# Optimization experiments

Hardware: AMD Instinct MI355X
Metric: run time of the kernel (lower is better)

## Reference

```python
import jax, jax.numpy as jnp
import numpy as np
from jax import lax

LAG = 0.5  # lag_constant

def setup_inputs() -> dict:
    key = jax.random.key(0)
    ks = jax.random.split(key, 8)
    B, T, D, H, O = 64, 512, 256, 1024, 256
    return {
        "obs_seq": jax.random.normal(ks[0], (B, T, D), dtype=jnp.float32),
        "h0": jax.random.normal(ks[1], (B, H), dtype=jnp.float32),
        "W_in": jax.random.normal(ks[2], (H, D), dtype=jnp.float32) * (1.0 / np.sqrt(D)),
        "b_in": jax.random.normal(ks[3], (H,), dtype=jnp.float32) * 0.01,
        "W_h": jax.random.normal(ks[4], (H, H), dtype=jnp.float32) * (1.0 / np.sqrt(H)),
        "b_h": jax.random.normal(ks[5], (H,), dtype=jnp.float32) * 0.01,
        "W_out": jax.random.normal(ks[6], (O, H), dtype=jnp.float32) * (1.0 / np.sqrt(H)),
        "b_out": jax.random.normal(ks[7], (O,), dtype=jnp.float32) * 0.01,
    }

def reference(obs_seq, h0, W_in, b_in, W_h, b_h, W_out, b_out):
    # obs_seq: [B, T, D]; scan over time with hard sequential dependency on h.
    def step(h, obs_t):  # h: [B,H], obs_t: [B,D]
        pre = obs_t @ W_in.T + b_in + h @ W_h.T + b_h
        h_new = LAG * jax.nn.relu(pre) + (1.0 - LAG) * h
        out = h_new @ W_out.T + b_out  # [B,O]
        return h_new, (out, h_new)

    obs_tbd = jnp.swapaxes(obs_seq, 0, 1)  # [T,B,D]
    _, (outs, hs) = lax.scan(step, h0, obs_tbd)
    # stack along seq_dim=1 as in the original
    return jnp.swapaxes(outs, 0, 1), jnp.swapaxes(hs, 0, 1)
```

## Files before the change

kernel.cpp:

```cpp
#include <hip/hip_runtime.h>
#include <cstddef>


static constexpr int Bb = 64;
static constexpr int Tt = 512;
static constexpr int Dd = 256;
static constexpr int Hh = 1024;
static constexpr int Oo = 256;

typedef __attribute__((ext_vector_type(8))) short bf16x8;
typedef __attribute__((ext_vector_type(4))) float f32x4;
typedef unsigned long long ull;

static __device__ __forceinline__ unsigned short f2b(float f) {
    unsigned int u = __float_as_uint(f);
    u = (u + 0x7fffu + ((u >> 16) & 1u)) >> 16;
    return (unsigned short)u;
}
static __device__ __forceinline__ ull pack4(float a, float b, float c, float d) {
    return (ull)f2b(a) | ((ull)f2b(b) << 16) | ((ull)f2b(c) << 32) | ((ull)f2b(d) << 48);
}

static __device__ __forceinline__ int hla_base(int r) {
    return ((r >> 5) << 7) + (((r >> 3) & 3) << 3) + (r & 7);
}
static __device__ __forceinline__ int hla_addr(int r, int m) {
    return hla_base(r) + (m << 5);
}

__global__ __launch_bounds__(256) void gemm_bt_kernel(const float* __restrict__ A,
                                                      const float* __restrict__ Bt,
                                                      const float* __restrict__ bias1,
                                                      const float* __restrict__ bias2,
                                                      float* __restrict__ C,
                                                      int M, int N, int K)
{
    __shared__ float As[128 * 17];
    __shared__ float Bs[128 * 17];
    const int tid = threadIdx.x;
    const int nTiles = N >> 7;
    const int mt = blockIdx.x / nTiles;
    const int nt = blockIdx.x - mt * nTiles;
    const int m0 = mt << 7, n0 = nt << 7;
    const int tx = tid & 15, ty = tid >> 4;

    const int row = tid >> 1;
    const int c8  = (tid & 1) << 3;

    float acc[8][8] = {};

    for (int kt = 0; kt < K; kt += 16) {
        const float4 a0 = *(const float4*)&A [(size_t)(m0 + row) * K + kt + c8];
        const float4 a1 = *(const float4*)&A [(size_t)(m0 + row) * K + kt + c8 + 4];
        const float4 b0 = *(const float4*)&Bt[(size_t)(n0 + row) * K + kt + c8];
        const float4 b1 = *(const float4*)&Bt[(size_t)(n0 + row) * K + kt + c8 + 4];
        __syncthreads();
        {
            const int ab = row * 17 + c8;
            As[ab + 0] = a0.x; As[ab + 1] = a0.y; As[ab + 2] = a0.z; As[ab + 3] = a0.w;
            As[ab + 4] = a1.x; As[ab + 5] = a1.y; As[ab + 6] = a1.z; As[ab + 7] = a1.w;
            Bs[ab + 0] = b0.x; Bs[ab + 1] = b0.y; Bs[ab + 2] = b0.z; Bs[ab + 3] = b0.w;
            Bs[ab + 4] = b1.x; Bs[ab + 5] = b1.y; Bs[ab + 6] = b1.z; Bs[ab + 7] = b1.w;
        }
        __syncthreads();
#pragma unroll
        for (int kk = 0; kk < 16; ++kk) {
            float af[8], bf[8];
#pragma unroll
            for (int i = 0; i < 8; ++i) af[i] = As[(ty * 8 + i) * 17 + kk];
#pragma unroll
            for (int j = 0; j < 4; ++j) bf[j] = Bs[(tx * 4 + j) * 17 + kk];
#pragma unroll
            for (int j = 0; j < 4; ++j) bf[4 + j] = Bs[(64 + tx * 4 + j) * 17 + kk];
#pragma unroll
            for (int i = 0; i < 8; ++i) {
#pragma unroll
                for (int j = 0; j < 8; ++j) {
                    acc[i][j] = fmaf(af[i], bf[j], acc[i][j]);
                }
            }
        }
    }

    float bs[8];
#pragma unroll
    for (int j = 0; j < 4; ++j) {
        const int n1 = n0 + tx * 4 + j;
        const int n2 = n0 + 64 + tx * 4 + j;
        bs[j]     = bias1[n1] + (bias2 ? bias2[n1] : 0.0f);
        bs[4 + j] = bias1[n2] + (bias2 ? bias2[n2] : 0.0f);
    }
#pragma unroll
    for (int i = 0; i < 8; ++i) {
        const int m = m0 + ty * 8 + i;
        float4 v0 = make_float4(acc[i][0] + bs[0], acc[i][1] + bs[1],
                                acc[i][2] + bs[2], acc[i][3] + bs[3]);
        float4 v1 = make_float4(acc[i][4] + bs[4], acc[i][5] + bs[5],
                                acc[i][6] + bs[6], acc[i][7] + bs[7]);
        *(float4*)&C[(size_t)m * N + n0 + tx * 4]      = v0;
        *(float4*)&C[(size_t)m * N + n0 + 64 + tx * 4] = v1;
    }
}

__global__ __launch_bounds__(512, 2) void rnn_kernel(float* __restrict__ Xhs,
                                                     const float* __restrict__ h0,
                                                     const float* __restrict__ Wh,
                                                     ull* __restrict__ hx)
{
    __shared__ short hlA[2][32 * 128];

    const int tid  = threadIdx.x;
    const int bid  = blockIdx.x;
    const int team = bid & 15;
    const int wg   = bid >> 4;
    const int r0   = wg << 7;
    const int b0   = team << 2;

    const int lane = tid & 63;
    const int wv   = tid >> 6;

    bf16x8 wfrag[32];
    {
        const float* wrow = Wh + (size_t)(r0 + wv * 16 + (lane & 15)) * Hh + ((lane >> 4) << 3);
#pragma unroll
        for (int s = 0; s < 32; ++s) {
            const float4 lo = *(const float4*)(wrow + s * 32);
            const float4 hi = *(const float4*)(wrow + s * 32 + 4);
            bf16x8 w;
            w[0] = (short)f2b(lo.x); w[1] = (short)f2b(lo.y);
            w[2] = (short)f2b(lo.z); w[3] = (short)f2b(lo.w);
            w[4] = (short)f2b(hi.x); w[5] = (short)f2b(hi.y);
            w[6] = (short)f2b(hi.z); w[7] = (short)f2b(hi.w);
            wfrag[s] = w;
        }
    }

#pragma unroll
    for (int it = 0; it < 2; ++it) {
        const int idx = it * 512 + tid;
        const int b   = idx >> 8;
        const int k0  = (idx & 255) << 2;
        const float4 v = *(const float4*)&h0[(size_t)(b0 + b) * Hh + k0];
        *(ull*)&hlA[0][hla_addr(k0, b)] = pack4(v.x, v.y, v.z, v.w);
    }

    const int npair = (tid < 384) ? 2 : 1;
    int soff[2], sbase[2];
#pragma unroll
    for (int j = 0; j < 2; ++j) {
        int q = tid + j * 512; if (q >= 896) q = 0;
        const int wr = q >> 7;
        const int rl = q & 127;
        const int wi = wr + ((wr >= wg) ? 1 : 0);
        soff[j]  = (wi << 8) + (rl << 1);
        sbase[j] = hla_base((wi << 7) + rl);
    }

    const bool ex    = (lane < 16);
    const int  exrow = r0 + wv * 16 + lane;
    const int  sb    = hla_base(exrow);
    float hprev[4] = {0.f, 0.f, 0.f, 0.f};
    if (ex) {
#pragma unroll
        for (int i = 0; i < 4; ++i)
            hprev[i] = h0[(size_t)(b0 + i) * Hh + exrow];
    }
    __syncthreads();

    const int aoff = (lane & 3) * 32 + ((lane >> 4) << 3);

    for (int t = 0; t < Tt; ++t) {
        const short* hc = hlA[t & 1];
        short*       hn = hlA[(t + 1) & 1];

        float xr[4] = {0.f, 0.f, 0.f, 0.f};
        if (ex) {
#pragma unroll
            for (int i = 0; i < 4; ++i)
                xr[i] = Xhs[((size_t)(b0 + i) * Tt + t) * Hh + exrow];
        }

        f32x4 acc0 = {0.f, 0.f, 0.f, 0.f}, acc1 = acc0, acc2 = acc0, acc3 = acc0;
#pragma unroll
        for (int s = 0; s < 32; s += 4) {
            acc0 = __builtin_amdgcn_mfma_f32_16x16x32_bf16(
                       *(const bf16x8*)(hc + (s + 0) * 128 + aoff), wfrag[s + 0], acc0, 0, 0, 0);
            acc1 = __builtin_amdgcn_mfma_f32_16x16x32_bf16(
                       *(const bf16x8*)(hc + (s + 1) * 128 + aoff), wfrag[s + 1], acc1, 0, 0, 0);
            acc2 = __builtin_amdgcn_mfma_f32_16x16x32_bf16(
                       *(const bf16x8*)(hc + (s + 2) * 128 + aoff), wfrag[s + 2], acc2, 0, 0, 0);
            acc3 = __builtin_amdgcn_mfma_f32_16x16x32_bf16(
                       *(const bf16x8*)(hc + (s + 3) * 128 + aoff), wfrag[s + 3], acc3, 0, 0, 0);
        }
        const f32x4 accs01 = acc0 + acc1;
        const f32x4 accs23 = acc2 + acc3;
        const f32x4 acc    = accs01 + accs23;

        float hnew[4] = {0.f, 0.f, 0.f, 0.f};
        unsigned short hb[4] = {0, 0, 0, 0};
        if (ex) {
#pragma unroll
            for (int i = 0; i < 4; ++i) {
                const float pre = acc[i] + xr[i];
                hnew[i]  = 0.5f * fmaxf(pre, 0.0f) + 0.5f * hprev[i];
                hprev[i] = hnew[i];
                hb[i]    = f2b(hnew[i]);
            }
        }

        if (t + 1 < Tt) {
            ull* __restrict__ slab =
                hx + (size_t)(((t + 1) & 1) * 16 + team) * (8 * 256);
            const unsigned want = (unsigned)(t + 1);

            if (ex) {
                const ull tg = (ull)want << 48;
                const ull wlo = (ull)hb[0] | ((ull)hb[1] << 16)
                              | ((ull)hb[2] << 32) | tg;
                const ull whi = (ull)hb[3] | tg;
                const int pw = (wg << 8) + ((wv * 16 + lane) << 1);
                __hip_atomic_store(&slab[pw],     wlo,
                                   __ATOMIC_RELAXED, __HIP_MEMORY_SCOPE_AGENT);
                __hip_atomic_store(&slab[pw + 1], whi,
                                   __ATOMIC_RELAXED, __HIP_MEMORY_SCOPE_AGENT);
                hn[sb]      = (short)hb[0];
                hn[sb + 32] = (short)hb[1];
                hn[sb + 64] = (short)hb[2];
                hn[sb + 96] = (short)hb[3];
            }

            {
                bool dn[4] = {false, false, npair < 2, npair < 2};
                int  rem = npair << 1;
                while (rem > 0) {
                    ull v[4];
#pragma unroll
                    for (int j = 0; j < 4; ++j) {
                        if (!dn[j])
                            v[j] = __hip_atomic_load(&slab[soff[j >> 1] + (j & 1)],
                                                     __ATOMIC_RELAXED,
                                                     __HIP_MEMORY_SCOPE_AGENT);
                    }
#pragma unroll
                    for (int j = 0; j < 4; ++j) {
                        if (!dn[j] && (unsigned)(v[j] >> 48) == want) {
                            dn[j] = true; --rem;
                            const int base = sbase[j >> 1];
                            if ((j & 1) == 0) {
                                hn[base]      = (short)(v[j] & 0xffffu);
                                hn[base + 32] = (short)((v[j] >> 16) & 0xffffu);
                                hn[base + 64] = (short)((v[j] >> 32) & 0xffffu);
                            } else {
                                hn[base + 96] = (short)(v[j] & 0xffffu);
                            }
                        }
                    }
                }
            }

            if (ex) {
#pragma unroll
                for (int i = 0; i < 4; ++i)
                    Xhs[((size_t)(b0 + i) * Tt + t) * Hh + exrow] = hnew[i];
            }
            __syncthreads();
        } else {
            if (ex) {
#pragma unroll
                for (int i = 0; i < 4; ++i)
                    Xhs[((size_t)(b0 + i) * Tt + t) * Hh + exrow] = hnew[i];
            }
        }
    }
}

extern "C" void kernel_launch(void* const* d_in, const int* in_sizes, int n_in,
                              void* d_out, int out_size, void* d_ws, size_t ws_size,
                              hipStream_t stream)
{
    (void)in_sizes; (void)n_in; (void)out_size; (void)ws_size;

    const float* obs  = (const float*)d_in[0];
    const float* h0   = (const float*)d_in[1];
    const float* Win  = (const float*)d_in[2];
    const float* bin  = (const float*)d_in[3];
    const float* Wh   = (const float*)d_in[4];
    const float* bh   = (const float*)d_in[5];
    const float* Wout = (const float*)d_in[6];
    const float* bout = (const float*)d_in[7];

    float* outs = (float*)d_out;
    float* hs   = outs + (size_t)Bb * Tt * Oo;

    ull* hx = (ull*)d_ws;

    gemm_bt_kernel<<<(Bb * Tt / 128) * (Hh / 128), 256, 0, stream>>>(
        obs, Win, bin, bh, hs, Bb * Tt, Hh, Dd);

    rnn_kernel<<<128, 512, 0, stream>>>(hs, h0, Wh, hx);

    gemm_bt_kernel<<<(Bb * Tt / 128) * (Oo / 128), 256, 0, stream>>>(
        hs, Wout, bout, nullptr, outs, Bb * Tt, Oo, Hh);
}
```

Baseline: 1.680 ms.

## Replace FP32 FMA GEMMs with bf16 MFMA kernels, split-bf16 for input projection

Replaces the scalar FP32 tiled GEMM used for the input projection and the output projection with a matrix-core kernel built on mfma_f32_16x16x32_bf16. Operands are converted to bf16 as they are staged into shared memory. The input projection (SPLIT=1) keeps near-FP32 accuracy by splitting each value into high and low bf16 parts and issuing three MFMAs per tile. The output projection uses plain bf16, which lowers precision in exchange for less compute. The output stores change from float4 writes to scalar per-lane writes in the MFMA layout, which may reduce store efficiency.

```diff
diff --git a/kernel.cpp b/kernel.cpp
--- a/kernel.cpp
+++ b/kernel.cpp
@@ -17,6 +17,9 @@
     u = (u + 0x7fffu + ((u >> 16) & 1u)) >> 16;
     return (unsigned short)u;
 }
+static __device__ __forceinline__ float b2f(unsigned short b) {
+    return __uint_as_float(((unsigned int)b) << 16);
+}
 static __device__ __forceinline__ ull pack4(float a, float b, float c, float d) {
     return (ull)f2b(a) | ((ull)f2b(b) << 16) | ((ull)f2b(c) << 32) | ((ull)f2b(d) << 48);
 }
@@ -28,77 +31,123 @@
     return hla_base(r) + (m << 5);
 }
 
-__global__ __launch_bounds__(256) void gemm_bt_kernel(const float* __restrict__ A,
-                                                      const float* __restrict__ Bt,
-                                                      const float* __restrict__ bias1,
-                                                      const float* __restrict__ bias2,
-                                                      float* __restrict__ C,
-                                                      int M, int N, int K)
+template <int SPLIT>
+__global__ __launch_bounds__(256) void gemm_mfma_bt(const float* __restrict__ A,
+                                                    const float* __restrict__ Bt,
+                                                    const float* __restrict__ bias1,
+                                                    const float* __restrict__ bias2,
+                                                    float* __restrict__ C,
+                                                    int M, int N, int K)
 {
-    __shared__ float As[128 * 17];
-    __shared__ float Bs[128 * 17];
+    __shared__ short Ah[128 * 40];
+    __shared__ short Bh[128 * 40];
+    __shared__ short Al[SPLIT ? 128 * 40 : 8];
+    __shared__ short Bl[SPLIT ? 128 * 40 : 8];
+
     const int tid = threadIdx.x;
     const int nTiles = N >> 7;
     const int mt = blockIdx.x / nTiles;
     const int nt = blockIdx.x - mt * nTiles;
     const int m0 = mt << 7, n0 = nt << 7;
-    const int tx = tid & 15, ty = tid >> 4;
-
-    const int row = tid >> 1;
-    const int c8  = (tid & 1) << 3;
-
-    float acc[8][8] = {};
-
-    for (int kt = 0; kt < K; kt += 16) {
-        const float4 a0 = *(const float4*)&A [(size_t)(m0 + row) * K + kt + c8];
-        const float4 a1 = *(const float4*)&A [(size_t)(m0 + row) * K + kt + c8 + 4];
-        const float4 b0 = *(const float4*)&Bt[(size_t)(n0 + row) * K + kt + c8];
-        const float4 b1 = *(const float4*)&Bt[(size_t)(n0 + row) * K + kt + c8 + 4];
+
+    const int lane = tid & 63;
+    const int wv   = tid >> 6;
+    const int wr   = (wv >> 1) << 6;
+    const int wc   = (wv & 1) << 6;
+    const int fr   = lane & 15;
+    const int fk   = (lane >> 4) << 3;
+
+    const int srow = tid >> 1;
+    const int scg  = (tid & 1) << 4;
+
+    const float* arow = A  + (size_t)(m0 + srow) * K + scg;
+    const float* brow = Bt + (size_t)(n0 + srow) * K + scg;
+
+    f32x4 acc[4][4] = {};
+
+    for (int kt = 0; kt < K; kt += 32) {
+        float4 av[4], bv[4];
+#pragma unroll
+        for (int j = 0; j < 4; ++j) {
+            av[j] = *(const float4*)(arow + kt + 4 * j);
+            bv[j] = *(const float4*)(brow + kt + 4 * j);
+        }
         __syncthreads();
         {
-            const int ab = row * 17 + c8;
-            As[ab + 0] = a0.x; As[ab + 1] = a0.y; As[ab + 2] = a0.z; As[ab + 3] = a0.w;
-            As[ab + 4] = a1.x; As[ab + 5] = a1.y; As[ab + 6] = a1.z; As[ab + 7] = a1.w;
-            Bs[ab + 0] = b0.x; Bs[ab + 1] = b0.y; Bs[ab + 2] = b0.z; Bs[ab + 3] = b0.w;
-            Bs[ab + 4] = b1.x; Bs[ab + 5] = b1.y; Bs[ab + 6] = b1.z; Bs[ab + 7] = b1.w;
+            short ahl[16], bhl[16], all_[16], bll[16];
+#pragma unroll
+            for (int j = 0; j < 4; ++j) {
+#pragma unroll
+                for (int e = 0; e < 4; ++e) {
+                    const float fa = (&av[j].x)[e];
+                    const float fb = (&bv[j].x)[e];
+                    const unsigned short ha = f2b(fa);
+                    const unsigned short hb = f2b(fb);
+                    ahl[j * 4 + e] = (short)ha;
+                    bhl[j * 4 + e] = (short)hb;
+                    if constexpr (SPLIT) {
+                        all_[j * 4 + e] = (short)f2b(fa - b2f(ha));
+                        bll[j * 4 + e] = (short)f2b(fb - b2f(hb));
+                    }
+                }
+            }
+            const int sb = srow * 40 + scg;
+            *(bf16x8*)&Ah[sb]     = *(bf16x8*)&ahl[0];
+            *(bf16x8*)&Ah[sb + 8] = *(bf16x8*)&ahl[8];
+            *(bf16x8*)&Bh[sb]     = *(bf16x8*)&bhl[0];
+            *(bf16x8*)&Bh[sb + 8] = *(bf16x8*)&bhl[8];
+            if constexpr (SPLIT) {
+                *(bf16x8*)&Al[sb]     = *(bf16x8*)&all_[0];
+                *(bf16x8*)&Al[sb + 8] = *(bf16x8*)&all_[8];
+                *(bf16x8*)&Bl[sb]     = *(bf16x8*)&bll[0];
+                *(bf16x8*)&Bl[sb + 8] = *(bf16x8*)&bll[8];
+            }
         }
         __syncthreads();
-#pragma unroll
-        for (int kk = 0; kk < 16; ++kk) {
-            float af[8], bf[8];
-#pragma unroll
-            for (int i = 0; i < 8; ++i) af[i] = As[(ty * 8 + i) * 17 + kk];
-#pragma unroll
-            for (int j = 0; j < 4; ++j) bf[j] = Bs[(tx * 4 + j) * 17 + kk];
-#pragma unroll
-            for (int j = 0; j < 4; ++j) bf[4 + j] = Bs[(64 + tx * 4 + j) * 17 + kk];
-#pragma unroll
-            for (int i = 0; i < 8; ++i) {
-#pragma unroll
-                for (int j = 0; j < 8; ++j) {
-                    acc[i][j] = fmaf(af[i], bf[j], acc[i][j]);
+        bf16x8 ah[4], bh_[4], al[4], bl[4];
+#pragma unroll
+        for (int i = 0; i < 4; ++i) {
+            ah[i]  = *(const bf16x8*)&Ah[(wr + i * 16 + fr) * 40 + fk];
+            bh_[i] = *(const bf16x8*)&Bh[(wc + i * 16 + fr) * 40 + fk];
+            if constexpr (SPLIT) {
+                al[i] = *(const bf16x8*)&Al[(wr + i * 16 + fr) * 40 + fk];
+                bl[i] = *(const bf16x8*)&Bl[(wc + i * 16 + fr) * 40 + fk];
+            }
+        }
+#pragma unroll
+        for (int mi = 0; mi < 4; ++mi) {
+#pragma unroll
+            for (int ni = 0; ni < 4; ++ni) {
+                acc[mi][ni] = __builtin_amdgcn_mfma_f32_16x16x32_bf16(
+                                  ah[mi], bh_[ni], acc[mi][ni], 0, 0, 0);
+                if constexpr (SPLIT) {
+                    acc[mi][ni] = __builtin_amdgcn_mfma_f32_16x16x32_bf16(
+                                      ah[mi], bl[ni], acc[mi][ni], 0, 0, 0);
+                    acc[mi][ni] = __builtin_amdgcn_mfma_f32_16x16x32_bf16(
+                                      al[mi], bh_[ni], acc[mi][ni], 0, 0, 0);
                 }
             }
         }
     }
 
-    float bs[8];
-#pragma unroll
-    for (int j = 0; j < 4; ++j) {
-        const int n1 = n0 + tx * 4 + j;
-        const int n2 = n0 + 64 + tx * 4 + j;
-        bs[j]     = bias1[n1] + (bias2 ? bias2[n1] : 0.0f);
-        bs[4 + j] = bias1[n2] + (bias2 ? bias2[n2] : 0.0f);
-    }
-#pragma unroll
-    for (int i = 0; i < 8; ++i) {
-        const int m = m0 + ty * 8 + i;
-        float4 v0 = make_float4(acc[i][0] + bs[0], acc[i][1] + bs[1],
-                                acc[i][2] + bs[2], acc[i][3] + bs[3]);
-        float4 v1 = make_float4(acc[i][4] + bs[4], acc[i][5] + bs[5],
-                                acc[i][6] + bs[6], acc[i][7] + bs[7]);
-        *(float4*)&C[(size_t)m * N + n0 + tx * 4]      = v0;
-        *(float4*)&C[(size_t)m * N + n0 + 64 + tx * 4] = v1;
+    float bsv[4];
+#pragma unroll
+    for (int ni = 0; ni < 4; ++ni) {
+        const int col = n0 + wc + ni * 16 + fr;
+        bsv[ni] = bias1[col] + (bias2 ? bias2[col] : 0.0f);
+    }
+#pragma unroll
+    for (int mi = 0; mi < 4; ++mi) {
+#pragma unroll
+        for (int i = 0; i < 4; ++i) {
+            const int m = m0 + wr + mi * 16 + ((lane >> 4) << 2) + i;
+            float* crow = C + (size_t)m * N;
+#pragma unroll
+            for (int ni = 0; ni < 4; ++ni) {
+                const int col = n0 + wc + ni * 16 + fr;
+                crow[col] = acc[mi][ni][i] + bsv[ni];
+            }
+        }
     }
 }
 
@@ -294,11 +343,11 @@
 
     ull* hx = (ull*)d_ws;
 
-    gemm_bt_kernel<<<(Bb * Tt / 128) * (Hh / 128), 256, 0, stream>>>(
+    gemm_mfma_bt<1><<<(Bb * Tt / 128) * (Hh / 128), 256, 0, stream>>>(
         obs, Win, bin, bh, hs, Bb * Tt, Hh, Dd);
 
     rnn_kernel<<<128, 512, 0, stream>>>(hs, h0, Wh, hx);
 
-    gemm_bt_kernel<<<(Bb * Tt / 128) * (Oo / 128), 256, 0, stream>>>(
+    gemm_mfma_bt<0><<<(Bb * Tt / 128) * (Oo / 128), 256, 0, stream>>>(
         hs, Wout, bout, nullptr, outs, Bb * Tt, Oo, Hh);
 }
```

New measurement: 1.345 ms. 20.0% less time.
